# Kernel tuning notes

Measured on AMD Instinct MI355X. Metric: run time of the kernel, lower is better.

The kernel has to match this reference:

```python
import jax, jax.numpy as jnp
import numpy as np
import math

B, N, D, H = 16, 1024, 1024, 8
HD = D // H
SCALE = 1.0 / math.sqrt(D // 8)
NEG = -1e30


def setup_inputs() -> dict:
    key = jax.random.key(0)
    ks = jax.random.split(key, 10)
    s = 0.02
    return {
        "x": jax.random.normal(ks[0], (B, N, D), dtype=jnp.float32),
        "x_mask": jax.random.randint(ks[1], (B, N), 0, 2, dtype=jnp.int32),
        "Wq": jax.random.normal(ks[2], (H, D, HD), dtype=jnp.float32) * s,
        "bq": jnp.zeros((H, HD), dtype=jnp.float32),
        "Wk": jax.random.normal(ks[3], (H, D, HD), dtype=jnp.float32) * s,
        "bk": jnp.zeros((H, HD), dtype=jnp.float32),
        "Wv": jax.random.normal(ks[4], (H, D, HD), dtype=jnp.float32) * s,
        "bv": jnp.zeros((H, HD), dtype=jnp.float32),
        "Wfc": jax.random.normal(ks[5], (D, D), dtype=jnp.float32) * s,
        "bfc": jnp.zeros((D,), dtype=jnp.float32),
    }


def reference(x, x_mask, Wq, bq, Wk, bk, Wv, bv, Wfc, bfc):
    # per-head projections, stacked: [B, H, N, HD]
    q = jnp.einsum("bnd,hde->bhne", x, Wq) + bq[None, :, None, :]
    k = jnp.einsum("bnd,hde->bhne", x, Wk) + bk[None, :, None, :]
    v = jnp.einsum("bnd,hde->bhne", x, Wv) + bv[None, :, None, :]
    # pairwise padding mask: mask & mask^T  ->  outer product for 0/1 values
    m = x_mask.astype(x.dtype)  # [B, N]
    mask = m[:, :, None] * m[:, None, :]  # [B, N, N]
    scores = jnp.einsum("bhne,bhme->bhnm", q, k) * SCALE  # [B, H, N, N]
    scores = scores * mask[:, None] + NEG * (1.0 - mask[:, None])
    attn = jax.nn.softmax(scores, axis=-1)
    o = jnp.einsum("bhnm,bhme->bhne", attn, v)  # [B, H, N, HD]
    # concat heads along feature dim (head order preserved)
    o = jnp.transpose(o, (0, 2, 1, 3)).reshape(B, N, D)
    out = o @ Wfc + bfc  # final fc; F.dropout result is discarded in source
    return out
```

## Files before the change

kernel.cpp:

```cpp
#include <hip/hip_runtime.h>
#include <hip/hip_bf16.h>
#include <math.h>

#define BN 1024
#define DD 1024
#define NB 16
#define NH 8
#define HDIM 128

typedef __attribute__((ext_vector_type(8))) short bf16x8;
typedef __attribute__((ext_vector_type(4))) float f32x4;
typedef __attribute__((ext_vector_type(4))) unsigned short ushort4v;

#define DEV __device__ __forceinline__

DEV unsigned short f2bf(float f) {
  unsigned u = __float_as_uint(f);
  u = (u + 0x7fffu + ((u >> 16) & 1u)) >> 16;
  return (unsigned short)u;
}

DEV f32x4 mfma16(bf16x8 a, bf16x8 b, f32x4 c) {
  return __builtin_amdgcn_mfma_f32_16x16x32_bf16(a, b, c, 0, 0, 0);
}

DEV void async16(const unsigned short* g, unsigned short* l) {
  __builtin_amdgcn_global_load_lds(
      (const __attribute__((address_space(1))) unsigned short*)g,
      (__attribute__((address_space(3))) unsigned short*)l, 16, 0, 0);
}

__global__ __launch_bounds__(256) void prep_kernel(
    const float* __restrict__ x, const float* __restrict__ Wq,
    const float* __restrict__ Wk, const float* __restrict__ Wv,
    const float* __restrict__ Wfc, unsigned short* __restrict__ x_bf,
    unsigned short* __restrict__ wqkvT, unsigned short* __restrict__ wfcT) {
  __shared__ float tile[32][33];
  const int bx = blockIdx.x, tid = threadIdx.x;
  if (bx < 16384) {
    int i = bx * 256 + tid;
    const float4* p = (const float4*)x;
    float4 v = p[i];
    ushort4v o;
    o[0] = f2bf(v.x); o[1] = f2bf(v.y); o[2] = f2bf(v.z); o[3] = f2bf(v.w);
    *(ushort4v*)(x_bf + (size_t)i * 4) = o;
    return;
  }
  const int tx = tid & 31, ty = tid >> 5;
  if (bx < 19456) {
    int idx = bx - 16384;
    int k0 = (idx & 31) * 32, e0 = ((idx >> 5) & 3) * 32, z = idx >> 7;
    int which = z >> 3, h = z & 7;
    const float* in = (which == 0 ? Wq : (which == 1 ? Wk : Wv)) + (size_t)h * DD * HDIM;
#pragma unroll
    for (int i = 0; i < 4; ++i)
      tile[ty + i * 8][tx] = in[(size_t)(k0 + ty + i * 8) * HDIM + e0 + tx];
    __syncthreads();
    int rowbase = which * 1024 + h * 128 + e0;
#pragma unroll
    for (int i = 0; i < 4; ++i)
      wqkvT[(size_t)(rowbase + ty + i * 8) * DD + k0 + tx] = f2bf(tile[tx][ty + i * 8]);
  } else {
    int idx = bx - 19456;
    int d0 = (idx & 31) * 32, c0 = (idx >> 5) * 32;
#pragma unroll
    for (int i = 0; i < 4; ++i)
      tile[ty + i * 8][tx] = Wfc[(size_t)(d0 + ty + i * 8) * DD + c0 + tx];
    __syncthreads();
#pragma unroll
    for (int i = 0; i < 4; ++i)
      wfcT[(size_t)(c0 + ty + i * 8) * DD + d0 + tx] = f2bf(tile[tx][ty + i * 8]);
  }
}

template <int MODE>
__global__ __launch_bounds__(256, 3) void gemm128_kernel(
    const unsigned short* __restrict__ A, const unsigned short* __restrict__ Bt,
    const float* __restrict__ bias0, const float* __restrict__ bias1,
    const float* __restrict__ bias2, unsigned short* __restrict__ out0,
    unsigned short* __restrict__ out1, unsigned short* __restrict__ out2,
    float* __restrict__ outf) {
  __shared__ unsigned short as[128 * 64];
  __shared__ unsigned short bs[128 * 64];
  const int tid = threadIdx.x;
  const int wave = tid >> 6, lane = tid & 63, quad = lane >> 4, l15 = lane & 15;
  const int wr = wave >> 1, wc = wave & 1;
  const int m0 = (blockIdx.x & 127) << 7, n0 = (blockIdx.x >> 7) << 7;
  f32x4 acc[4][4] = {};

  const int srow = wave * 32 + (lane >> 3);
  const int gch = ((lane & 7) - (lane >> 3)) & 7;
  const unsigned short* ag = A + (size_t)(m0 + srow) * 1024 + gch * 8;
  const unsigned short* bg = Bt + (size_t)(n0 + srow) * 1024 + gch * 8;
  unsigned short* as_w = as + wave * 32 * 64;
  unsigned short* bs_w = bs + wave * 32 * 64;

  for (int kb = 0; kb < 1024; kb += 64) {
#pragma unroll
    for (int i = 0; i < 4; ++i) {
      async16(ag + kb + i * 8 * 1024, as_w + i * 512);
      async16(bg + kb + i * 8 * 1024, bs_w + i * 512);
    }
    __syncthreads();
#pragma unroll
    for (int ks = 0; ks < 2; ++ks) {
      const int sl = ((quad + ks * 4 + l15) & 7) * 8;
      bf16x8 af[4], bfr[4];
#pragma unroll
      for (int mt = 0; mt < 4; ++mt)
        af[mt] = *(const bf16x8*)(as + (wr * 64 + mt * 16 + l15) * 64 + sl);
#pragma unroll
      for (int nt = 0; nt < 4; ++nt)
        bfr[nt] = *(const bf16x8*)(bs + (wc * 64 + nt * 16 + l15) * 64 + sl);
#pragma unroll
      for (int mt = 0; mt < 4; ++mt)
#pragma unroll
        for (int nt = 0; nt < 4; ++nt)
          acc[mt][nt] = mfma16(af[mt], bfr[nt], acc[mt][nt]);
    }
    __syncthreads();
  }

  if constexpr (MODE == 0) {
    const int seg = n0 >> 10;
#pragma unroll
    for (int mt = 0; mt < 4; ++mt) {
      int mb = m0 + wr * 64 + mt * 16 + quad * 4;
      int bb = mb >> 10, nn = mb & 1023;
#pragma unroll
      for (int nt = 0; nt < 4; ++nt) {
        int c = n0 + wc * 64 + nt * 16 + l15;
        int cc = c & 1023;
        int h = cc >> 7, e = cc & 127;
        if (seg == 2) {
          float bias = bias2[cc];
          ushort4v pv;
#pragma unroll
          for (int r = 0; r < 4; ++r) pv[r] = f2bf(acc[mt][nt][r] + bias);
          *(ushort4v*)(out2 + ((size_t)(bb * NH + h) * HDIM + e) * BN + nn) = pv;
        } else {
          const float* bp = (seg == 0) ? bias0 : bias1;
          unsigned short* op = (seg == 0) ? out0 : out1;
          float bias = bp[cc];
#pragma unroll
          for (int r = 0; r < 4; ++r)
            op[(((size_t)bb * NH + h) * BN + (nn + r)) * HDIM + e] =
                f2bf(acc[mt][nt][r] + bias);
        }
      }
    }
  } else {
#pragma unroll
    for (int mt = 0; mt < 4; ++mt) {
      int mb = m0 + wr * 64 + mt * 16 + quad * 4;
#pragma unroll
      for (int nt = 0; nt < 4; ++nt) {
        int c = n0 + wc * 64 + nt * 16 + l15;
        float bias = bias0[c];
#pragma unroll
        for (int r = 0; r < 4; ++r)
          outf[(size_t)(mb + r) * DD + c] = acc[mt][nt][r] + bias;
      }
    }
  }
}

__global__ __launch_bounds__(256, 2) void flash_attn_kernel(
    const unsigned short* __restrict__ Q, const unsigned short* __restrict__ Kk,
    const unsigned short* __restrict__ Vt, const int* __restrict__ xmask,
    unsigned short* __restrict__ O) {
  __shared__ unsigned short k_s[64 * 128];
  __shared__ unsigned short v_s[2][128 * 64];
  __shared__ unsigned short p_s[128 * 72];
  __shared__ float l_s[2][128];

  const float CL2E = 0.08838834764831845f * 1.44269504088896f;

  const int tid = threadIdx.x;
  const int w = tid >> 6, lane = tid & 63, quad = lane >> 4, l15 = lane & 15;
  const int wq = w >> 1, wk = w & 1;
  const int lin = blockIdx.x;
  const int bh = lin & 127, qb = lin >> 7;
  const int b = bh >> 3, h = bh & 7;
  const int q0 = qb * 128;
  const unsigned short* qp = Q + ((size_t)bh * BN + q0) * HDIM;
  const unsigned short* kp = Kk + (size_t)bh * BN * HDIM;
  const unsigned short* vp = Vt + (size_t)bh * HDIM * BN;
  const int* xm_b = xmask + b * BN;

  bf16x8 qf[4][4];
#pragma unroll
  for (int mt = 0; mt < 4; ++mt)
#pragma unroll
    for (int ks = 0; ks < 4; ++ks)
      qf[mt][ks] = *(const bf16x8*)(qp + (wq * 64 + mt * 16 + l15) * HDIM + ks * 32 + quad * 8);

  int rowm_bits = 0;
#pragma unroll
  for (int mt = 0; mt < 4; ++mt)
#pragma unroll
    for (int r = 0; r < 4; ++r)
      rowm_bits |= (xm_b[q0 + wq * 64 + mt * 16 + quad * 4 + r] ? 1 : 0) << (mt * 4 + r);

  const int krow = lane >> 4;
  const int vrow = lane >> 3;
  const int vch = ((lane & 7) - vrow) & 7;

  float l_lane[4][4] = {};
  f32x4 o_acc[4][4] = {};

#pragma unroll
  for (int i = 0; i < 4; ++i) {
    int rmod = i * 4 + krow;
    int g = ((lane & 15) - rmod) & 15;
    async16(kp + (size_t)(w * 16 + rmod) * HDIM + g * 8, k_s + (w * 16 + i * 4) * 128);
    int e = w * 32 + i * 8 + vrow;
    async16(vp + (size_t)e * BN + vch * 8, v_s[0] + (w * 32 + i * 8) * 64);
  }

  for (int it = 0; it < 16; ++it) {
    const int kb = it * 64;
    int cm0 = xm_b[kb + wk * 32 + l15];
    int cm1 = xm_b[kb + wk * 32 + 16 + l15];
    __syncthreads();

    f32x4 s[4][2] = {};
#pragma unroll
    for (int ks = 0; ks < 4; ++ks) {
      const int sl = ((ks * 4 + quad + l15) & 15) * 8;
      bf16x8 b0 = *(const bf16x8*)(k_s + (wk * 32 + l15) * 128 + sl);
      bf16x8 b1 = *(const bf16x8*)(k_s + (wk * 32 + 16 + l15) * 128 + sl);
#pragma unroll
      for (int mt = 0; mt < 4; ++mt) {
        s[mt][0] = mfma16(qf[mt][ks], b0, s[mt][0]);
        s[mt][1] = mfma16(qf[mt][ks], b1, s[mt][1]);
      }
    }

#pragma unroll
    for (int mt = 0; mt < 4; ++mt)
#pragma unroll
      for (int nt = 0; nt < 2; ++nt) {
        int cmv = nt ? cm1 : cm0;
#pragma unroll
        for (int r = 0; r < 4; ++r) {
          float xs = s[mt][nt][r] * CL2E;
          float t = cmv ? xs : -60.0f;
          int rb = (rowm_bits >> (mt * 4 + r)) & 1;
          float e2 = rb ? t : 0.0f;
          float p = __builtin_amdgcn_exp2f(e2);
          l_lane[mt][r] += p;
          p_s[(wq * 64 + mt * 16 + quad * 4 + r) * 72 + wk * 32 + nt * 16 + l15] = f2bf(p);
        }
      }

    __syncthreads();

    {
      const int kn = (kb + 64) & (BN - 1);
      unsigned short* vb_next = v_s[(it + 1) & 1];
#pragma unroll
      for (int i = 0; i < 4; ++i) {
        int rmod = i * 4 + krow;
        int g = ((lane & 15) - rmod) & 15;
        async16(kp + (size_t)(kn + w * 16 + rmod) * HDIM + g * 8,
                k_s + (w * 16 + i * 4) * 128);
        int e = w * 32 + i * 8 + vrow;
        async16(vp + (size_t)e * BN + kn + vch * 8, vb_next + (w * 32 + i * 8) * 64);
      }
    }

    const unsigned short* vb = v_s[it & 1];
#pragma unroll
    for (int ks2 = 0; ks2 < 2; ++ks2) {
      const int sl = ((ks2 * 4 + quad + l15) & 7) * 8;
      bf16x8 pa[4];
#pragma unroll
      for (int mt = 0; mt < 4; ++mt)
        pa[mt] = *(const bf16x8*)(p_s + (wq * 64 + mt * 16 + l15) * 72 + ks2 * 32 + quad * 8);
#pragma unroll
      for (int et = 0; et < 4; ++et) {
        bf16x8 bv = *(const bf16x8*)(vb + (wk * 64 + et * 16 + l15) * 64 + sl);
#pragma unroll
        for (int mt = 0; mt < 4; ++mt)
          o_acc[mt][et] = mfma16(pa[mt], bv, o_acc[mt][et]);
      }
    }
  }

#pragma unroll
  for (int mt = 0; mt < 4; ++mt)
#pragma unroll
    for (int r = 0; r < 4; ++r) {
      float l = l_lane[mt][r];
#pragma unroll
      for (int off = 1; off < 16; off <<= 1) l += __shfl_xor(l, off, 64);
      if (l15 == 0) l_s[wk][wq * 64 + mt * 16 + quad * 4 + r] = l;
    }
  __syncthreads();

#pragma unroll
  for (int mt = 0; mt < 4; ++mt)
#pragma unroll
    for (int r = 0; r < 4; ++r) {
      int rl = wq * 64 + mt * 16 + quad * 4 + r;
      float inv = 1.0f / (l_s[0][rl] + l_s[1][rl]);
      int row = q0 + rl;
#pragma unroll
      for (int et = 0; et < 4; ++et) {
        int col = h * HDIM + wk * 64 + et * 16 + l15;
        O[((size_t)b * BN + row) * DD + col] = f2bf(o_acc[mt][et][r] * inv);
      }
    }
}

extern "C" void kernel_launch(void* const* d_in, const int* in_sizes, int n_in,
                              void* d_out, int out_size, void* d_ws, size_t ws_size,
                              hipStream_t stream) {
  const float* x = (const float*)d_in[0];
  const int* xmask = (const int*)d_in[1];
  const float* Wq = (const float*)d_in[2];
  const float* bq = (const float*)d_in[3];
  const float* Wk = (const float*)d_in[4];
  const float* bk = (const float*)d_in[5];
  const float* Wv = (const float*)d_in[6];
  const float* bv = (const float*)d_in[7];
  const float* Wfc = (const float*)d_in[8];
  const float* bfc = (const float*)d_in[9];
  float* out = (float*)d_out;

  char* ws = (char*)d_ws;
  unsigned short* x_bf  = (unsigned short*)(ws);
  unsigned short* wqkvT = (unsigned short*)(ws + 33554432);
  unsigned short* wfcT  = (unsigned short*)(ws + 39845888);
  unsigned short* q_bf  = (unsigned short*)(ws + 41943040);
  unsigned short* k_bf  = (unsigned short*)(ws + 75497472);
  unsigned short* vT_bf = (unsigned short*)(ws + 109051904);
  unsigned short* o_bf  = (unsigned short*)(ws + 142606336);

  prep_kernel<<<dim3(20480), dim3(256), 0, stream>>>(x, Wq, Wk, Wv, Wfc, x_bf, wqkvT, wfcT);

  gemm128_kernel<0><<<dim3(3072), dim3(256), 0, stream>>>(
      x_bf, wqkvT, bq, bk, bv, q_bf, k_bf, vT_bf, nullptr);

  flash_attn_kernel<<<dim3(1024), dim3(256), 0, stream>>>(q_bf, k_bf, vT_bf, xmask, o_bf);

  gemm128_kernel<1><<<dim3(1024), dim3(256), 0, stream>>>(
      o_bf, wfcT, bfc, nullptr, nullptr, nullptr, nullptr, nullptr, out);
}
```

Measured before the change: 395.7 us.

## Replace 128x128 GEMM with double-buffered 256x256 pipelined GEMM and block swizzle

Rewrites the projection and output GEMMs as a 256x256-tile, 512-thread kernel that double-buffers shared memory. The next k-tile's async loads are interleaved with four MFMA quadrant phases, using explicit vmcnt/lgkmcnt waits, barriers and setprio. It also adds a block-index swizzle for L2 locality. The aim is to raise arithmetic intensity and hide global-load latency behind MFMA work, at the cost of more LDS (128KB) and register pressure, which limits occupancy.

```diff
diff --git a/kernel.cpp b/kernel.cpp
--- a/kernel.cpp
+++ b/kernel.cpp
@@ -74,92 +74,182 @@
 }
 
 template <int MODE>
-__global__ __launch_bounds__(256, 3) void gemm128_kernel(
+__global__ __launch_bounds__(512, 2) void gemm256_kernel(
     const unsigned short* __restrict__ A, const unsigned short* __restrict__ Bt,
     const float* __restrict__ bias0, const float* __restrict__ bias1,
     const float* __restrict__ bias2, unsigned short* __restrict__ out0,
     unsigned short* __restrict__ out1, unsigned short* __restrict__ out2,
     float* __restrict__ outf) {
-  __shared__ unsigned short as[128 * 64];
-  __shared__ unsigned short bs[128 * 64];
+  __shared__ unsigned short As[2][256 * 64];
+  __shared__ unsigned short Bs[2][256 * 64];
   const int tid = threadIdx.x;
-  const int wave = tid >> 6, lane = tid & 63, quad = lane >> 4, l15 = lane & 15;
-  const int wr = wave >> 1, wc = wave & 1;
-  const int m0 = (blockIdx.x & 127) << 7, n0 = (blockIdx.x >> 7) << 7;
-  f32x4 acc[4][4] = {};
-
-  const int srow = wave * 32 + (lane >> 3);
-  const int gch = ((lane & 7) - (lane >> 3)) & 7;
+  const int w = tid >> 6, lane = tid & 63, quad = lane >> 4, l15 = lane & 15;
+  const int wr = w >> 2, wc = w & 3;
+
+  constexpr int NBN = (MODE == 0) ? 12 : 4;
+  constexpr int CPX = (MODE == 0) ? 96 : 32;
+  const int bid = blockIdx.x;
+  const int swz = (bid & 7) * CPX + (bid >> 3);
+  const int mblk = swz / NBN, nblk = swz - mblk * NBN;
+  const int m0 = mblk << 8, n0 = nblk << 8;
+
+  const int srow = tid >> 3;
+  const int gch = ((tid & 7) - srow) & 7;
   const unsigned short* ag = A + (size_t)(m0 + srow) * 1024 + gch * 8;
   const unsigned short* bg = Bt + (size_t)(n0 + srow) * 1024 + gch * 8;
-  unsigned short* as_w = as + wave * 32 * 64;
-  unsigned short* bs_w = bs + wave * 32 * 64;
-
-  for (int kb = 0; kb < 1024; kb += 64) {
-#pragma unroll
-    for (int i = 0; i < 4; ++i) {
-      async16(ag + kb + i * 8 * 1024, as_w + i * 512);
-      async16(bg + kb + i * 8 * 1024, bs_w + i * 512);
-    }
-    __syncthreads();
-#pragma unroll
-    for (int ks = 0; ks < 2; ++ks) {
-      const int sl = ((quad + ks * 4 + l15) & 7) * 8;
-      bf16x8 af[4], bfr[4];
-#pragma unroll
-      for (int mt = 0; mt < 4; ++mt)
-        af[mt] = *(const bf16x8*)(as + (wr * 64 + mt * 16 + l15) * 64 + sl);
-#pragma unroll
-      for (int nt = 0; nt < 4; ++nt)
-        bfr[nt] = *(const bf16x8*)(bs + (wc * 64 + nt * 16 + l15) * 64 + sl);
-#pragma unroll
-      for (int mt = 0; mt < 4; ++mt)
-#pragma unroll
-        for (int nt = 0; nt < 4; ++nt)
-          acc[mt][nt] = mfma16(af[mt], bfr[nt], acc[mt][nt]);
-    }
-    __syncthreads();
+  const int wbase = w * 512;
+
+  const int sl0 = ((quad + l15) & 7) * 8;
+  const int sl1 = ((quad + l15 + 4) & 7) * 8;
+
+  f32x4 acc[8][4] = {};
+  bf16x8 af[4][2];
+  bf16x8 bfr[4][2];
+
+  async16(ag, &As[0][0] + wbase);
+  async16(ag + 64 * 1024, &As[0][64 * 64] + wbase);
+  async16(bg, &Bs[0][0] + wbase);
+  async16(bg + 64 * 1024, &Bs[0][64 * 64] + wbase);
+  async16(bg + 128 * 1024, &Bs[0][128 * 64] + wbase);
+  async16(bg + 192 * 1024, &Bs[0][192 * 64] + wbase);
+  async16(ag + 128 * 1024, &As[0][128 * 64] + wbase);
+  async16(ag + 192 * 1024, &As[0][192 * 64] + wbase);
+  asm volatile("s_waitcnt vmcnt(4)" ::: "memory");
+  __builtin_amdgcn_s_barrier();
+
+  for (int t = 0; t < 16; ++t) {
+    const int cur = t & 1;
+    const unsigned short* ac = &As[cur][0];
+    const unsigned short* bc = &Bs[cur][0];
+    unsigned short* an = &As[cur ^ 1][0];
+    unsigned short* bn = &Bs[cur ^ 1][0];
+    const int kb2 = ((t + 1) & 15) * 64;
+
+#pragma unroll
+    for (int mt = 0; mt < 4; ++mt) {
+      const unsigned short* rp = ac + (wr * 16 + mt * 32 + l15) * 64;
+      af[mt][0] = *(const bf16x8*)(rp + sl0);
+      af[mt][1] = *(const bf16x8*)(rp + sl1);
+    }
+#pragma unroll
+    for (int nt = 0; nt < 2; ++nt) {
+      const unsigned short* rp = bc + (wc * 16 + nt * 64 + l15) * 64;
+      bfr[nt][0] = *(const bf16x8*)(rp + sl0);
+      bfr[nt][1] = *(const bf16x8*)(rp + sl1);
+    }
+    async16(ag + kb2, an + wbase);
+    async16(ag + kb2 + 64 * 1024, an + 64 * 64 + wbase);
+    asm volatile("s_waitcnt vmcnt(4)" ::: "memory");
+    __builtin_amdgcn_s_barrier();
+    asm volatile("s_waitcnt lgkmcnt(0)" ::: "memory");
+    __builtin_amdgcn_s_setprio(1);
+#pragma unroll
+    for (int mt = 0; mt < 4; ++mt)
+#pragma unroll
+      for (int nt = 0; nt < 2; ++nt) {
+        acc[mt][nt] = mfma16(af[mt][0], bfr[nt][0], acc[mt][nt]);
+        acc[mt][nt] = mfma16(af[mt][1], bfr[nt][1], acc[mt][nt]);
+      }
+    __builtin_amdgcn_s_setprio(0);
+    __builtin_amdgcn_s_barrier();
+
+#pragma unroll
+    for (int nt = 0; nt < 2; ++nt) {
+      const unsigned short* rp = bc + (wc * 16 + 128 + nt * 64 + l15) * 64;
+      bfr[2 + nt][0] = *(const bf16x8*)(rp + sl0);
+      bfr[2 + nt][1] = *(const bf16x8*)(rp + sl1);
+    }
+    async16(bg + kb2, bn + wbase);
+    async16(bg + kb2 + 64 * 1024, bn + 64 * 64 + wbase);
+    asm volatile("s_waitcnt vmcnt(4)" ::: "memory");
+    __builtin_amdgcn_s_barrier();
+    asm volatile("s_waitcnt lgkmcnt(0)" ::: "memory");
+    __builtin_amdgcn_s_setprio(1);
+#pragma unroll
+    for (int mt = 0; mt < 4; ++mt)
+#pragma unroll
+      for (int nt = 0; nt < 2; ++nt) {
+        acc[mt][2 + nt] = mfma16(af[mt][0], bfr[2 + nt][0], acc[mt][2 + nt]);
+        acc[mt][2 + nt] = mfma16(af[mt][1], bfr[2 + nt][1], acc[mt][2 + nt]);
+      }
+    __builtin_amdgcn_s_setprio(0);
+    __builtin_amdgcn_s_barrier();
+
+#pragma unroll
+    for (int mt = 0; mt < 4; ++mt) {
+      const unsigned short* rp = ac + (wr * 16 + 128 + mt * 32 + l15) * 64;
+      af[mt][0] = *(const bf16x8*)(rp + sl0);
+      af[mt][1] = *(const bf16x8*)(rp + sl1);
+    }
+    async16(bg + kb2 + 128 * 1024, bn + 128 * 64 + wbase);
+    async16(bg + kb2 + 192 * 1024, bn + 192 * 64 + wbase);
+    __builtin_amdgcn_s_barrier();
+    asm volatile("s_waitcnt lgkmcnt(0)" ::: "memory");
+    __builtin_amdgcn_s_setprio(1);
+#pragma unroll
+    for (int mt = 0; mt < 4; ++mt)
+#pragma unroll
+      for (int nt = 0; nt < 2; ++nt) {
+        acc[4 + mt][2 + nt] = mfma16(af[mt][0], bfr[2 + nt][0], acc[4 + mt][2 + nt]);
+        acc[4 + mt][2 + nt] = mfma16(af[mt][1], bfr[2 + nt][1], acc[4 + mt][2 + nt]);
+      }
+    __builtin_amdgcn_s_setprio(0);
+    __builtin_amdgcn_s_barrier();
+
+    async16(ag + kb2 + 128 * 1024, an + 128 * 64 + wbase);
+    async16(ag + kb2 + 192 * 1024, an + 192 * 64 + wbase);
+    asm volatile("s_waitcnt vmcnt(4)" ::: "memory");
+    __builtin_amdgcn_s_barrier();
+    __builtin_amdgcn_s_setprio(1);
+#pragma unroll
+    for (int mt = 0; mt < 4; ++mt)
+#pragma unroll
+      for (int nt = 0; nt < 2; ++nt) {
+        acc[4 + mt][nt] = mfma16(af[mt][0], bfr[nt][0], acc[4 + mt][nt]);
+        acc[4 + mt][nt] = mfma16(af[mt][1], bfr[nt][1], acc[4 + mt][nt]);
+      }
+    __builtin_amdgcn_s_setprio(0);
+    __builtin_amdgcn_s_barrier();
   }
 
   if constexpr (MODE == 0) {
     const int seg = n0 >> 10;
-#pragma unroll
-    for (int mt = 0; mt < 4; ++mt) {
-      int mb = m0 + wr * 64 + mt * 16 + quad * 4;
+    const float* bp = (seg == 0) ? bias0 : (seg == 1 ? bias1 : bias2);
+#pragma unroll
+    for (int ai = 0; ai < 8; ++ai) {
+      int mb = m0 + wr * 16 + ai * 32 + quad * 4;
       int bb = mb >> 10, nn = mb & 1023;
 #pragma unroll
       for (int nt = 0; nt < 4; ++nt) {
-        int c = n0 + wc * 64 + nt * 16 + l15;
+        int c = n0 + wc * 16 + nt * 64 + l15;
         int cc = c & 1023;
         int h = cc >> 7, e = cc & 127;
+        float bias = bp[cc];
         if (seg == 2) {
-          float bias = bias2[cc];
           ushort4v pv;
 #pragma unroll
-          for (int r = 0; r < 4; ++r) pv[r] = f2bf(acc[mt][nt][r] + bias);
+          for (int r = 0; r < 4; ++r) pv[r] = f2bf(acc[ai][nt][r] + bias);
           *(ushort4v*)(out2 + ((size_t)(bb * NH + h) * HDIM + e) * BN + nn) = pv;
         } else {
-          const float* bp = (seg == 0) ? bias0 : bias1;
           unsigned short* op = (seg == 0) ? out0 : out1;
-          float bias = bp[cc];
 #pragma unroll
           for (int r = 0; r < 4; ++r)
             op[(((size_t)bb * NH + h) * BN + (nn + r)) * HDIM + e] =
-                f2bf(acc[mt][nt][r] + bias);
+                f2bf(acc[ai][nt][r] + bias);
         }
       }
     }
   } else {
 #pragma unroll
-    for (int mt = 0; mt < 4; ++mt) {
-      int mb = m0 + wr * 64 + mt * 16 + quad * 4;
+    for (int ai = 0; ai < 8; ++ai) {
+      int mb = m0 + wr * 16 + ai * 32 + quad * 4;
 #pragma unroll
       for (int nt = 0; nt < 4; ++nt) {
-        int c = n0 + wc * 64 + nt * 16 + l15;
+        int c = n0 + wc * 16 + nt * 64 + l15;
         float bias = bias0[c];
 #pragma unroll
         for (int r = 0; r < 4; ++r)
-          outf[(size_t)(mb + r) * DD + c] = acc[mt][nt][r] + bias;
+          outf[(size_t)(mb + r) * DD + c] = acc[ai][nt][r] + bias;
       }
     }
   }
@@ -340,11 +430,11 @@
 
   prep_kernel<<<dim3(20480), dim3(256), 0, stream>>>(x, Wq, Wk, Wv, Wfc, x_bf, wqkvT, wfcT);
 
-  gemm128_kernel<0><<<dim3(3072), dim3(256), 0, stream>>>(
+  gemm256_kernel<0><<<dim3(768), dim3(512), 0, stream>>>(
       x_bf, wqkvT, bq, bk, bv, q_bf, k_bf, vT_bf, nullptr);
 
   flash_attn_kernel<<<dim3(1024), dim3(256), 0, stream>>>(q_bf, k_bf, vT_bf, xmask, o_bf);
 
-  gemm128_kernel<1><<<dim3(1024), dim3(256), 0, stream>>>(
+  gemm256_kernel<1><<<dim3(256), dim3(512), 0, stream>>>(
       o_bf, wfcT, bfc, nullptr, nullptr, nullptr, nullptr, nullptr, out);
 }
```

Result: no change. 393.4 us (-0.6%).

## Rewrite flash attention with 32x32 MFMA and register-resident P via permlane swap

Applied to the files above, without the earlier changes.

The attention kernel switches from 16x16x32 to 32x32x16 bf16 MFMA, with each wave owning 32 query rows across the full key block. It computes S transposed (K as the A operand), so the probabilities can be packed to bf16 with v_cvt_pk and rearranged with v_permlane32_swap into PV operands in registers. This removes the LDS round trip for P and the partial row-sum reduction across waves. It also builds the key mask with a ballot and raises wave priority during the PV MFMAs. In exchange it relies on gfx950-specific instructions and uses more accumulator registers per wave.

```diff
diff --git a/kernel.cpp b/kernel.cpp
--- a/kernel.cpp
+++ b/kernel.cpp
@@ -10,6 +10,7 @@
 
 typedef __attribute__((ext_vector_type(8))) short bf16x8;
 typedef __attribute__((ext_vector_type(4))) float f32x4;
+typedef __attribute__((ext_vector_type(16))) float f32x16;
 typedef __attribute__((ext_vector_type(4))) unsigned short ushort4v;
 
 #define DEV __device__ __forceinline__
@@ -24,10 +25,28 @@
   return __builtin_amdgcn_mfma_f32_16x16x32_bf16(a, b, c, 0, 0, 0);
 }
 
+DEV f32x16 mfma32(bf16x8 a, bf16x8 b, f32x16 c) {
+  return __builtin_amdgcn_mfma_f32_32x32x16_bf16(a, b, c, 0, 0, 0);
+}
+
 DEV void async16(const unsigned short* g, unsigned short* l) {
   __builtin_amdgcn_global_load_lds(
       (const __attribute__((address_space(1))) unsigned short*)g,
       (__attribute__((address_space(3))) unsigned short*)l, 16, 0, 0);
+}
+
+DEV unsigned cvtpk(float lo, float hi_) {
+  unsigned r;
+  asm("v_cvt_pk_bf16_f32 %0, %1, %2" : "=v"(r) : "v"(lo), "v"(hi_));
+  return r;
+}
+DEV void swap32(unsigned& a, unsigned& b) {
+  asm volatile("v_permlane32_swap_b32 %0, %1" : "+v"(a), "+v"(b));
+}
+DEV bf16x8 mk8(unsigned a, unsigned b, unsigned c, unsigned d) {
+  union { unsigned u[4]; bf16x8 v; } t;
+  t.u[0] = a; t.u[1] = b; t.u[2] = c; t.u[3] = d;
+  return t.v;
 }
 
 __global__ __launch_bounds__(256) void prep_kernel(
@@ -171,14 +190,13 @@
     unsigned short* __restrict__ O) {
   __shared__ unsigned short k_s[64 * 128];
   __shared__ unsigned short v_s[2][128 * 64];
-  __shared__ unsigned short p_s[128 * 72];
-  __shared__ float l_s[2][128];
+  __shared__ float l_s[128];
 
   const float CL2E = 0.08838834764831845f * 1.44269504088896f;
 
   const int tid = threadIdx.x;
-  const int w = tid >> 6, lane = tid & 63, quad = lane >> 4, l15 = lane & 15;
-  const int wq = w >> 1, wk = w & 1;
+  const int w = tid >> 6, lane = tid & 63;
+  const int l31 = lane & 31, hi = lane >> 5;
   const int lin = blockIdx.x;
   const int bh = lin & 127, qb = lin >> 7;
   const int b = bh >> 3, h = bh & 7;
@@ -188,26 +206,19 @@
   const unsigned short* vp = Vt + (size_t)bh * HDIM * BN;
   const int* xm_b = xmask + b * BN;
 
-  bf16x8 qf[4][4];
-#pragma unroll
-  for (int mt = 0; mt < 4; ++mt)
-#pragma unroll
-    for (int ks = 0; ks < 4; ++ks)
-      qf[mt][ks] = *(const bf16x8*)(qp + (wq * 64 + mt * 16 + l15) * HDIM + ks * 32 + quad * 8);
-
-  int rowm_bits = 0;
-#pragma unroll
-  for (int mt = 0; mt < 4; ++mt)
-#pragma unroll
-    for (int r = 0; r < 4; ++r)
-      rowm_bits |= (xm_b[q0 + wq * 64 + mt * 16 + quad * 4 + r] ? 1 : 0) << (mt * 4 + r);
+  bf16x8 qf[8];
+#pragma unroll
+  for (int dk = 0; dk < 8; ++dk)
+    qf[dk] = *(const bf16x8*)(qp + (size_t)(w * 32 + l31) * HDIM + dk * 16 + hi * 8);
+
+  const int rm = xm_b[q0 + w * 32 + l31];
 
   const int krow = lane >> 4;
   const int vrow = lane >> 3;
   const int vch = ((lane & 7) - vrow) & 7;
 
-  float l_lane[4][4] = {};
-  f32x4 o_acc[4][4] = {};
+  float l_lane = 0.0f;
+  f32x16 o_acc[4] = {};
 
 #pragma unroll
   for (int i = 0; i < 4; ++i) {
@@ -220,39 +231,52 @@
 
   for (int it = 0; it < 16; ++it) {
     const int kb = it * 64;
-    int cm0 = xm_b[kb + wk * 32 + l15];
-    int cm1 = xm_b[kb + wk * 32 + 16 + l15];
-    __syncthreads();
-
-    f32x4 s[4][2] = {};
-#pragma unroll
-    for (int ks = 0; ks < 4; ++ks) {
-      const int sl = ((ks * 4 + quad + l15) & 15) * 8;
-      bf16x8 b0 = *(const bf16x8*)(k_s + (wk * 32 + l15) * 128 + sl);
-      bf16x8 b1 = *(const bf16x8*)(k_s + (wk * 32 + 16 + l15) * 128 + sl);
-#pragma unroll
-      for (int mt = 0; mt < 4; ++mt) {
-        s[mt][0] = mfma16(qf[mt][ks], b0, s[mt][0]);
-        s[mt][1] = mfma16(qf[mt][ks], b1, s[mt][1]);
-      }
-    }
-
-#pragma unroll
-    for (int mt = 0; mt < 4; ++mt)
-#pragma unroll
-      for (int nt = 0; nt < 2; ++nt) {
-        int cmv = nt ? cm1 : cm0;
-#pragma unroll
-        for (int r = 0; r < 4; ++r) {
-          float xs = s[mt][nt][r] * CL2E;
-          float t = cmv ? xs : -60.0f;
-          int rb = (rowm_bits >> (mt * 4 + r)) & 1;
-          float e2 = rb ? t : 0.0f;
-          float p = __builtin_amdgcn_exp2f(e2);
-          l_lane[mt][r] += p;
-          p_s[(wq * 64 + mt * 16 + quad * 4 + r) * 72 + wk * 32 + nt * 16 + l15] = f2bf(p);
-        }
-      }
+    const unsigned long long mb = __ballot(xm_b[kb + lane] != 0);
+    const unsigned long long mbh = mb >> (4 * hi);
+
+    __syncthreads();
+
+    f32x16 s0 = {}, s1 = {};
+#pragma unroll
+    for (int dk = 0; dk < 8; ++dk) {
+      const int cc = (2 * dk + hi + (l31 & 15)) & 15;
+      bf16x8 k0 = *(const bf16x8*)(k_s + (size_t)l31 * 128 + cc * 8);
+      bf16x8 k1 = *(const bf16x8*)(k_s + (size_t)(32 + l31) * 128 + cc * 8);
+      s0 = mfma32(k0, qf[dk], s0);
+      s1 = mfma32(k1, qf[dk], s1);
+    }
+
+    float p0[16], p1[16];
+#pragma unroll
+    for (int r = 0; r < 16; ++r) {
+      const int sh = (r & 3) + 8 * (r >> 2);
+      float x0 = s0[r] * CL2E, x1 = s1[r] * CL2E;
+      float t0 = ((mbh >> sh) & 1) ? x0 : -60.0f;
+      float t1 = ((mbh >> (sh + 32)) & 1) ? x1 : -60.0f;
+      float e0 = rm ? t0 : 0.0f;
+      float e1 = rm ? t1 : 0.0f;
+      p0[r] = __builtin_amdgcn_exp2f(e0);
+      p1[r] = __builtin_amdgcn_exp2f(e1);
+      l_lane += p0[r] + p1[r];
+    }
+
+    bf16x8 pa0, pa1, pa2, pa3;
+    {
+      unsigned a0 = cvtpk(p0[0], p0[1]), a1 = cvtpk(p0[2], p0[3]);
+      unsigned a2 = cvtpk(p0[4], p0[5]), a3 = cvtpk(p0[6], p0[7]);
+      unsigned b0 = cvtpk(p0[8], p0[9]), b1 = cvtpk(p0[10], p0[11]);
+      unsigned b2 = cvtpk(p0[12], p0[13]), b3 = cvtpk(p0[14], p0[15]);
+      swap32(a0, a2); swap32(a1, a3); swap32(b0, b2); swap32(b1, b3);
+      pa0 = mk8(a0, a1, a2, a3);
+      pa1 = mk8(b0, b1, b2, b3);
+      unsigned c0 = cvtpk(p1[0], p1[1]), c1 = cvtpk(p1[2], p1[3]);
+      unsigned c2 = cvtpk(p1[4], p1[5]), c3 = cvtpk(p1[6], p1[7]);
+      unsigned d0 = cvtpk(p1[8], p1[9]), d1 = cvtpk(p1[10], p1[11]);
+      unsigned d2 = cvtpk(p1[12], p1[13]), d3 = cvtpk(p1[14], p1[15]);
+      swap32(c0, c2); swap32(c1, c3); swap32(d0, d2); swap32(d1, d3);
+      pa2 = mk8(c0, c1, c2, c3);
+      pa3 = mk8(d0, d1, d2, d3);
+    }
 
     __syncthreads();
 
@@ -271,47 +295,38 @@
     }
 
     const unsigned short* vb = v_s[it & 1];
-#pragma unroll
-    for (int ks2 = 0; ks2 < 2; ++ks2) {
-      const int sl = ((ks2 * 4 + quad + l15) & 7) * 8;
-      bf16x8 pa[4];
-#pragma unroll
-      for (int mt = 0; mt < 4; ++mt)
-        pa[mt] = *(const bf16x8*)(p_s + (wq * 64 + mt * 16 + l15) * 72 + ks2 * 32 + quad * 8);
-#pragma unroll
-      for (int et = 0; et < 4; ++et) {
-        bf16x8 bv = *(const bf16x8*)(vb + (wk * 64 + et * 16 + l15) * 64 + sl);
-#pragma unroll
-        for (int mt = 0; mt < 4; ++mt)
-          o_acc[mt][et] = mfma16(pa[mt], bv, o_acc[mt][et]);
-      }
-    }
-  }
-
-#pragma unroll
-  for (int mt = 0; mt < 4; ++mt)
-#pragma unroll
-    for (int r = 0; r < 4; ++r) {
-      float l = l_lane[mt][r];
-#pragma unroll
-      for (int off = 1; off < 16; off <<= 1) l += __shfl_xor(l, off, 64);
-      if (l15 == 0) l_s[wk][wq * 64 + mt * 16 + quad * 4 + r] = l;
-    }
+    __builtin_amdgcn_s_setprio(1);
+#pragma unroll
+    for (int et = 0; et < 4; ++et) {
+      const int row = et * 32 + l31;
+      const int cb = (hi + (row & 7)) & 7;
+      bf16x8 v0 = *(const bf16x8*)(vb + (size_t)row * 64 + ((cb + 0) & 7) * 8);
+      bf16x8 v1 = *(const bf16x8*)(vb + (size_t)row * 64 + ((cb + 2) & 7) * 8);
+      bf16x8 v2 = *(const bf16x8*)(vb + (size_t)row * 64 + ((cb + 4) & 7) * 8);
+      bf16x8 v3 = *(const bf16x8*)(vb + (size_t)row * 64 + ((cb + 6) & 7) * 8);
+      o_acc[et] = mfma32(pa0, v0, o_acc[et]);
+      o_acc[et] = mfma32(pa1, v1, o_acc[et]);
+      o_acc[et] = mfma32(pa2, v2, o_acc[et]);
+      o_acc[et] = mfma32(pa3, v3, o_acc[et]);
+    }
+    __builtin_amdgcn_s_setprio(0);
+  }
+
+  l_lane += __shfl_xor(l_lane, 32, 64);
+  if (hi == 0) l_s[w * 32 + l31] = l_lane;
   __syncthreads();
 
 #pragma unroll
-  for (int mt = 0; mt < 4; ++mt)
-#pragma unroll
-    for (int r = 0; r < 4; ++r) {
-      int rl = wq * 64 + mt * 16 + quad * 4 + r;
-      float inv = 1.0f / (l_s[0][rl] + l_s[1][rl]);
-      int row = q0 + rl;
-#pragma unroll
-      for (int et = 0; et < 4; ++et) {
-        int col = h * HDIM + wk * 64 + et * 16 + l15;
-        O[((size_t)b * BN + row) * DD + col] = f2bf(o_acc[mt][et][r] * inv);
-      }
-    }
+  for (int r = 0; r < 16; ++r) {
+    const int ql = (r & 3) + 8 * (r >> 2) + 4 * hi;
+    const float inv = 1.0f / l_s[w * 32 + ql];
+    const int row = q0 + w * 32 + ql;
+#pragma unroll
+    for (int et = 0; et < 4; ++et) {
+      const int col = h * HDIM + et * 32 + l31;
+      O[((size_t)b * BN + row) * DD + col] = f2bf(o_acc[et][r] * inv);
+    }
+  }
 }
 
 extern "C" void kernel_launch(void* const* d_in, const int* in_sizes, int n_in,
```

Result: no change. 395.0 us (-0.2%).
